# Kernel tuning notes

Measured on AMD Instinct MI355X. Metric: run time of the kernel, lower is better.

## Reference

```python
import jax, jax.numpy as jnp
import numpy as np

HEADS = 8
BN_EPS = 1e-5

def _bn(x2d, g, b):
    # torch BatchNorm1d in training mode: biased batch stats
    mu = x2d.mean(0)
    var = x2d.var(0)
    return (x2d - mu) * jax.lax.rsqrt(var + BN_EPS) * g + b

def _window_indices(H):
    # exclusive-end box coordinates, in the exact order of the torch loop
    m = H // 2
    r0, r1, c0, c1 = [], [], [], []
    for i in range(1, m + 1):
        wins = [(m - i, m + i + 1, m - i, m + i + 1),  # full square
                (m - i, m + 1,     m - i, m + i + 1),  # top half
                (m,     m + i + 1, m - i, m + i + 1),  # bottom half
                (m - i, m + i + 1, m - i, m + 1),      # left half
                (m - i, m + i + 1, m,     m + i + 1)]  # right half
        for a, b, c, d in wins:
            r0.append(a); r1.append(b); c0.append(c); c1.append(d)
    r0 = np.array(r0); r1 = np.array(r1); c0 = np.array(c0); c1 = np.array(c1)
    counts = ((r1 - r0) * (c1 - c0)).astype(np.float32)
    return r0, r1, c0, c1, counts

def _box_sums(P, r0, r1, c0, c1):
    # P: padded 2D prefix sum [B, C, H+1, H+1]; returns [B, C, K]
    return P[:, :, r1, c1] - P[:, :, r0, c1] - P[:, :, r1, c0] + P[:, :, r0, c0]

def _integral(img):
    return jnp.pad(jnp.cumsum(jnp.cumsum(img, axis=2), axis=3), ((0, 0), (0, 0), (1, 0), (1, 0)))

def setup_inputs() -> dict:
    key = jax.random.key(0)
    ks = jax.random.split(key, 8)
    B, Cin, H = 64, 512, 31
    C = 512  # heads * base_dim
    x = jax.random.normal(ks[0], (B, Cin, H, H), dtype=jnp.float32)
    w_v = jax.random.normal(ks[1], (Cin, C), dtype=jnp.float32) * 0.02
    w_k = jax.random.normal(ks[2], (Cin, C), dtype=jnp.float32) * 0.02
    w_fc = jax.random.normal(ks[3], (Cin + C, 512), dtype=jnp.float32) * 0.02
    z = lambda n: jnp.zeros((n,), jnp.float32)
    o = lambda n: jnp.ones((n,), jnp.float32)
    return {"x": x,
            "w_v": w_v, "b_v": z(C), "g_vn": o(C), "b_vn": z(C),
            "w_k": w_k, "b_k": z(C), "g_kn": o(C), "b_kn": z(C),
            "w_fc": w_fc, "b_fc": z(512), "g_fcn": o(512), "b_fcn": z(512)}

def reference(x, w_v, b_v, g_vn, b_vn, w_k, b_k, g_kn, b_kn, w_fc, b_fc, g_fcn, b_fcn):
    B, Cin, H, W = x.shape
    N = H * W
    C = w_v.shape[1]
    d = C // HEADS
    m = H // 2
    xt = x.reshape(B, Cin, N).transpose(0, 2, 1)       # [B, N, Cin]
    x0 = xt[:, N // 2, :]                              # [B, Cin] center pixel feature
    flat = xt.reshape(B * N, Cin)
    v = jax.nn.relu(_bn(flat @ w_v + b_v, g_vn, b_vn))
    v = v.reshape(B, N, C).transpose(0, 2, 1).reshape(B, C, H, H)
    k = _bn(flat @ w_k + b_k, g_kn, b_kn).reshape(B, N, HEADS, d).transpose(0, 2, 1, 3)  # [B,h,N,d]
    q = k[:, :, N // 2, :]                             # [B, h, d]
    attn = jax.nn.softmax(jnp.einsum('bhd,bhnd->bhn', q, k) * (d ** -0.5), axis=-1)      # [B,h,N]
    attn_full = jnp.broadcast_to(attn[:, :, None, :], (B, HEADS, d, N)).reshape(B, C, H, H)
    xw = attn_full * v                                 # attn-weighted values [B,C,H,H]
    eps = 1e-16
    r0, r1, c0, c1, counts = _window_indices(H)
    Px = _integral(xw)
    Pa = _integral(attn_full)
    mx = _box_sums(Px, r0, r1, c0, c1) / counts        # window means of xw   [B,C,K]
    ma = _box_sums(Pa, r0, r1, c0, c1) / counts        # window means of attn [B,C,K]
    y_win = (mx / (ma + eps)).transpose(0, 2, 1)       # [B, K, C]
    y = jnp.concatenate([xw[:, :, m, m][:, None, :], y_win], axis=1)  # [B, n, C]
    # F.normalize(p=2, dim=2)
    y = y / jnp.maximum(jnp.linalg.norm(y, axis=2, keepdims=True), 1e-12)
    n = y.shape[1]
    yy = jnp.concatenate([jnp.broadcast_to(x0[:, None, :], (B, n, Cin)), y], axis=-1)
    out = jax.nn.relu(_bn(yy.reshape(B * n, Cin + C) @ w_fc + b_fc, g_fcn, b_fcn))
    return out.reshape(B, n, -1)
```

## Files before the change

kernel.cpp:

```cpp
#include <hip/hip_runtime.h>
#include <stdint.h>

#define DEV __device__ __forceinline__

typedef __bf16 bf16x8 __attribute__((ext_vector_type(8)));
typedef unsigned short u16x8 __attribute__((ext_vector_type(8)));
typedef float f32x4 __attribute__((ext_vector_type(4)));

DEV uint16_t f2bf(float f) {
    union { float f; uint32_t u; } v; v.f = f;
    uint32_t r = v.u + 0x7fffu + ((v.u >> 16) & 1u);
    return (uint16_t)(r >> 16);
}
DEV float bf2f(uint16_t h) {
    union { uint32_t u; float f; } v; v.u = ((uint32_t)h) << 16;
    return v.f;
}

#if __has_builtin(__builtin_amdgcn_global_load_lds)
DEV void async16(const uint16_t* g, uint16_t* l) {
    __builtin_amdgcn_global_load_lds(
        (const __attribute__((address_space(1))) uint32_t*)g,
        (__attribute__((address_space(3))) uint32_t*)l, 16, 0, 0);
}
#else
DEV void async16(const uint16_t* g, uint16_t* l) {
    *(u16x8*)l = *(const u16x8*)g;
}
#endif

__global__ void k_convert_x(const float* __restrict__ x, uint16_t* __restrict__ xbt) {
    __shared__ float tile[32][33];
    int b = blockIdx.z;
    int n0 = blockIdx.x * 32;
    int c0 = blockIdx.y * 32;
    int tx = threadIdx.x, ty = threadIdx.y;
    #pragma unroll
    for (int i = 0; i < 4; ++i) {
        int c = c0 + ty + 8 * i;
        int n = n0 + tx;
        float v = 0.f;
        if (n < 961) v = x[((size_t)b * 512 + c) * 961 + n];
        tile[ty + 8 * i][tx] = v;
    }
    __syncthreads();
    #pragma unroll
    for (int i = 0; i < 4; ++i) {
        int n = n0 + ty + 8 * i;
        if (n < 961)
            xbt[((size_t)b * 961 + n) * 512 + c0 + tx] = f2bf(tile[tx][ty + 8 * i]);
    }
}

__global__ void k_convert_wvk(const float* __restrict__ wv, const float* __restrict__ wk,
                              uint16_t* __restrict__ wvkt) {
    int idx = blockIdx.x * 256 + threadIdx.x;
    int j = idx >> 9, k = idx & 511;
    float v = (j < 512) ? wv[(size_t)k * 512 + j] : wk[(size_t)k * 512 + (j - 512)];
    wvkt[idx] = f2bf(v);
}
__global__ void k_convert_wfc(const float* __restrict__ wfc, uint16_t* __restrict__ wfct) {
    int idx = blockIdx.x * 256 + threadIdx.x;
    int j = idx >> 10, k = idx & 1023;
    wfct[idx] = f2bf(wfc[(size_t)k * 512 + j]);
}

template<int K, int EPI>
__global__ __launch_bounds__(256, 2)
void k_gemm(const uint16_t* __restrict__ A, const uint16_t* __restrict__ Bt,
            int M_real,
            uint16_t* __restrict__ out_v, uint16_t* __restrict__ out_k,
            float* __restrict__ out_f,
            float* __restrict__ colsum, float* __restrict__ colsq)
{
    __shared__ __align__(16) uint16_t sbuf[8704];
    __shared__ float sStat[256];
    uint16_t* sA = sbuf;
    uint16_t* sB = sbuf + 4096;

    const int tid = threadIdx.x;
    const int wave = tid >> 6, lane = tid & 63;
    const int quad = lane >> 4, l16 = lane & 15;
    int m0, j0;
    if constexpr (EPI == 0) {
        int lin = blockIdx.x;
        int xcd = lin & 7, rest = lin >> 3;
        int jb = rest & 7, mhi = rest >> 3;
        int mb = mhi * 8 + xcd;
        if (mb >= 481) return;
        m0 = mb * 128; j0 = jb * 128;
    } else {
        m0 = blockIdx.y * 128; j0 = blockIdx.x * 128;
    }
    const int wm = wave >> 1, wj = wave & 1;

    const f32x4 fzero = {0.f, 0.f, 0.f, 0.f};
    f32x4 acc[4][4];
    #pragma unroll
    for (int i = 0; i < 4; ++i)
        #pragma unroll
        for (int j = 0; j < 4; ++j) acc[i][j] = fzero;

    const int c0 = tid;
    const int mA0 = c0 >> 2, kq0 = c0 & 3;
    const int c1 = tid + 256;
    const int mA1 = c1 >> 2, kq1 = c1 & 3;

    const int KT = K / 32;
    for (int kt = 0; kt < KT; ++kt) {
        const uint16_t* Ak = A + (size_t)m0 * K + kt * 32;
        const uint16_t* Bk = Bt + (size_t)j0 * K + kt * 32;
        async16(Ak + (size_t)mA0 * K + kq0 * 8, &sA[c0 * 8]);
        async16(Bk + (size_t)mA0 * K + kq0 * 8, &sB[c0 * 8]);
        async16(Ak + (size_t)mA1 * K + kq1 * 8, &sA[c1 * 8]);
        async16(Bk + (size_t)mA1 * K + kq1 * 8, &sB[c1 * 8]);
        __syncthreads();
        bf16x8 af[4], bfr[4];
        #pragma unroll
        for (int i = 0; i < 4; ++i) {
            int m = wm * 64 + i * 16 + l16;
            u16x8 r = *(const u16x8*)&sA[m * 32 + quad * 8];
            af[i] = __builtin_bit_cast(bf16x8, r);
        }
        #pragma unroll
        for (int j = 0; j < 4; ++j) {
            int jj = wj * 64 + j * 16 + l16;
            u16x8 r = *(const u16x8*)&sB[jj * 32 + quad * 8];
            bfr[j] = __builtin_bit_cast(bf16x8, r);
        }
        #pragma unroll
        for (int i = 0; i < 4; ++i)
            #pragma unroll
            for (int j = 0; j < 4; ++j)
                acc[i][j] = __builtin_amdgcn_mfma_f32_16x16x32_bf16(af[i], bfr[j], acc[i][j], 0, 0, 0);
        __syncthreads();
    }

    sStat[tid] = 0.f;
    __syncthreads();

    #pragma unroll
    for (int j = 0; j < 4; ++j) {
        const int col_local = wj * 64 + j * 16 + l16;
        const int jg = j0 + col_local;
        float ls = 0.f, lq = 0.f;
        #pragma unroll
        for (int i = 0; i < 4; ++i) {
            const int rbase = m0 + wm * 64 + i * 16 + quad * 4;
            #pragma unroll
            for (int reg = 0; reg < 4; ++reg) {
                const int r = rbase + reg;
                const float val = acc[i][j][reg];
                if (r < M_real) {
                    ls += val; lq += val * val;
                    if constexpr (EPI == 1) {
                        out_f[(size_t)r * 512 + jg] = val;
                    }
                }
            }
        }
        ls += __shfl_xor(ls, 16); lq += __shfl_xor(lq, 16);
        ls += __shfl_xor(ls, 32); lq += __shfl_xor(lq, 32);
        if (quad == 0) {
            atomicAdd(&sStat[col_local], ls);
            atomicAdd(&sStat[128 + col_local], lq);
        }
    }
    __syncthreads();
    if (tid < 128) atomicAdd(&colsum[j0 + tid], sStat[tid]);
    else           atomicAdd(&colsq[j0 + (tid & 127)], sStat[tid]);

    if constexpr (EPI == 0) {
        const int rr = tid & 127;
        const int cbase = tid >> 7;
        const int r = m0 + rr;
        const bool ok = r < M_real;
        const unsigned bb_ = (unsigned)r / 961u;
        const unsigned nn = (unsigned)r - bb_ * 961u;
        #pragma unroll
        for (int ch = 0; ch < 2; ++ch) {
            if (wj == ch) {
                #pragma unroll
                for (int j = 0; j < 4; ++j) {
                    const int c = j * 16 + l16;
                    #pragma unroll
                    for (int i = 0; i < 4; ++i) {
                        const int rloc = wm * 64 + i * 16 + quad * 4;
                        union { uint16_t h[4]; uint64_t u; } p;
                        #pragma unroll
                        for (int reg = 0; reg < 4; ++reg) p.h[reg] = f2bf(acc[i][j][reg]);
                        *(uint64_t*)&sbuf[c * 136 + rloc] = p.u;
                    }
                }
            }
            __syncthreads();
            #pragma unroll
            for (int it = 0; it < 32; ++it) {
                const int c = cbase + it * 2;
                const int jg = j0 + ch * 64 + c;
                const uint16_t hv = sbuf[c * 136 + rr];
                if (ok) {
                    if (jg < 512) out_v[((size_t)bb_ * 512 + jg) * 961 + nn] = hv;
                    else          out_k[((size_t)bb_ * 512 + (jg - 512)) * 961 + nn] = hv;
                }
            }
            __syncthreads();
        }
    }
}

__global__ void k_bnfin(const float* __restrict__ s, const float* __restrict__ q,
                        const float* __restrict__ g, const float* __restrict__ be,
                        float* __restrict__ a, float* __restrict__ b2, float invM) {
    int j = blockIdx.x * 256 + threadIdx.x;
    float mean = s[j] * invM;
    float var = q[j] * invM - mean * mean;
    float aa = g[j] * rsqrtf(var + 1e-5f);
    a[j] = aa;
    b2[j] = be[j] - mean * aa;
}

__global__ void k_attn(const uint16_t* __restrict__ kraw,
                       const float* __restrict__ avec, const float* __restrict__ bvec,
                       float* __restrict__ attn, float* __restrict__ maw)
{
    __shared__ float qa[64];
    __shared__ float s_qb;
    __shared__ float att[961];
    __shared__ float red[8];

    int bh = blockIdx.x;
    int b = bh >> 3, h = bh & 7;
    int tid = threadIdx.x;

    if (tid < 64) {
        int c = h * 64 + tid;
        float kr = bf2f(kraw[((size_t)b * 512 + c) * 961 + 480]);
        float a = avec[512 + c], bb = bvec[512 + c];
        float qv = kr * a + bb;
        qa[tid] = qv * a;
        float qb = qv * bb;
        for (int off = 32; off; off >>= 1) qb += __shfl_down(qb, off);
        if (tid == 0) s_qb = qb;
    }
    __syncthreads();

    float lg[4];
    float lmax = -1e30f;
    #pragma unroll
    for (int it = 0; it < 4; ++it) {
        int n = tid + it * 256;
        float dot = -1e30f;
        if (n < 961) {
            const uint16_t* kp = kraw + ((size_t)b * 512 + h * 64) * 961 + n;
            float acc = 0.f;
            #pragma unroll 16
            for (int dd = 0; dd < 64; ++dd)
                acc += qa[dd] * bf2f(kp[(size_t)dd * 961]);
            dot = (acc + s_qb) * 0.125f;
        }
        lg[it] = dot;
        lmax = fmaxf(lmax, dot);
    }
    for (int off = 32; off; off >>= 1) lmax = fmaxf(lmax, __shfl_xor(lmax, off));
    if ((tid & 63) == 0) red[tid >> 6] = lmax;
    __syncthreads();
    float bmax = fmaxf(fmaxf(red[0], red[1]), fmaxf(red[2], red[3]));

    float lsum = 0.f;
    #pragma unroll
    for (int it = 0; it < 4; ++it) {
        int n = tid + it * 256;
        if (n < 961) {
            float e = __expf(lg[it] - bmax);
            lg[it] = e;
            lsum += e;
        }
    }
    for (int off = 32; off; off >>= 1) lsum += __shfl_xor(lsum, off);
    if ((tid & 63) == 0) red[4 + (tid >> 6)] = lsum;
    __syncthreads();
    float inv = 1.f / (red[4] + red[5] + red[6] + red[7]);
    #pragma unroll
    for (int it = 0; it < 4; ++it) {
        int n = tid + it * 256;
        if (n < 961) {
            float v = lg[it] * inv;
            att[n] = v;
            attn[(size_t)bh * 961 + n] = v;
        }
    }
    __syncthreads();

    if (tid < 31) { float s = 0.f; for (int cc = 0; cc < 31; ++cc) { s += att[tid * 31 + cc]; att[tid * 31 + cc] = s; } }
    __syncthreads();
    if (tid < 31) { float s = 0.f; for (int rr = 0; rr < 31; ++rr) { s += att[rr * 31 + tid]; att[rr * 31 + tid] = s; } }
    __syncthreads();

    if (tid < 75) {
        int i = tid / 5 + 1, t = tid % 5;
        const int m = 15;
        int r0, r1, cc0, cc1;
        switch (t) {
            case 0: r0 = m - i; r1 = m + i + 1; cc0 = m - i; cc1 = m + i + 1; break;
            case 1: r0 = m - i; r1 = m + 1;     cc0 = m - i; cc1 = m + i + 1; break;
            case 2: r0 = m;     r1 = m + i + 1; cc0 = m - i; cc1 = m + i + 1; break;
            case 3: r0 = m - i; r1 = m + i + 1; cc0 = m - i; cc1 = m + 1;     break;
            default:r0 = m - i; r1 = m + i + 1; cc0 = m;     cc1 = m + i + 1; break;
        }
        auto S = [&](int r, int c) -> float { return (r < 0 || c < 0) ? 0.f : att[r * 31 + c]; };
        float box = S(r1 - 1, cc1 - 1) - S(r0 - 1, cc1 - 1) - S(r1 - 1, cc0 - 1) + S(r0 - 1, cc0 - 1);
        float cnt = (float)((r1 - r0) * (cc1 - cc0));
        maw[(size_t)bh * 75 + tid] = box / cnt;
    }
}

__global__ void k_winbox(const uint16_t* __restrict__ vraw,
                         const float* __restrict__ avec, const float* __restrict__ bvec,
                         const float* __restrict__ attn, const float* __restrict__ maw,
                         float* __restrict__ y)
{
    __shared__ float xw[961];
    __shared__ float s_center;
    int bc = blockIdx.x;
    int b = bc >> 9, c = bc & 511;
    int h = c >> 6;
    int tid = threadIdx.x;
    float a = avec[c], bb = bvec[c];
    const uint16_t* vp = vraw + (size_t)bc * 961;
    const float* ap = attn + (size_t)(b * 8 + h) * 961;
    for (int n = tid; n < 961; n += 128) {
        float v = fmaxf(bf2f(vp[n]) * a + bb, 0.f);
        xw[n] = v * ap[n];
    }
    __syncthreads();
    if (tid == 0) s_center = xw[480];
    __syncthreads();
    if (tid < 31) { float s = 0.f; for (int cc = 0; cc < 31; ++cc) { s += xw[tid * 31 + cc]; xw[tid * 31 + cc] = s; } }
    __syncthreads();
    if (tid < 31) { float s = 0.f; for (int rr = 0; rr < 31; ++rr) { s += xw[rr * 31 + tid]; xw[rr * 31 + tid] = s; } }
    __syncthreads();
    if (tid < 75) {
        int i = tid / 5 + 1, t = tid % 5;
        const int m = 15;
        int r0, r1, cc0, cc1;
        switch (t) {
            case 0: r0 = m - i; r1 = m + i + 1; cc0 = m - i; cc1 = m + i + 1; break;
            case 1: r0 = m - i; r1 = m + 1;     cc0 = m - i; cc1 = m + i + 1; break;
            case 2: r0 = m;     r1 = m + i + 1; cc0 = m - i; cc1 = m + i + 1; break;
            case 3: r0 = m - i; r1 = m + i + 1; cc0 = m - i; cc1 = m + 1;     break;
            default:r0 = m - i; r1 = m + i + 1; cc0 = m;     cc1 = m + i + 1; break;
        }
        auto S = [&](int r, int cc) -> float { return (r < 0 || cc < 0) ? 0.f : xw[r * 31 + cc]; };
        float box = S(r1 - 1, cc1 - 1) - S(r0 - 1, cc1 - 1) - S(r1 - 1, cc0 - 1) + S(r0 - 1, cc0 - 1);
        float cnt = (float)((r1 - r0) * (cc1 - cc0));
        float mx = box / cnt;
        float ma = maw[(size_t)(b * 8 + h) * 75 + tid];
        y[((size_t)b * 76 + 1 + tid) * 512 + c] = mx / (ma + 1e-16f);
    }
    if (tid == 96) y[((size_t)b * 76) * 512 + c] = s_center;
}

__global__ void k_build_yy(const float* __restrict__ y, const float* __restrict__ x,
                           uint16_t* __restrict__ yy)
{
    __shared__ float red[4];
    int row = blockIdx.x;
    int b = row / 76;
    int tid = threadIdx.x;
    const float* yp = y + (size_t)row * 512;
    float v0 = yp[tid], v1 = yp[tid + 256];
    float ss = v0 * v0 + v1 * v1;
    for (int off = 32; off; off >>= 1) ss += __shfl_xor(ss, off);
    if ((tid & 63) == 0) red[tid >> 6] = ss;
    __syncthreads();
    float tot = red[0] + red[1] + red[2] + red[3];
    float inv = 1.f / fmaxf(sqrtf(tot), 1e-12f);
    uint16_t* op = yy + (size_t)row * 1024;
    op[tid]           = f2bf(x[((size_t)b * 512 + tid) * 961 + 480]);
    op[tid + 256]     = f2bf(x[((size_t)b * 512 + tid + 256) * 961 + 480]);
    op[512 + tid]       = f2bf(v0 * inv);
    op[512 + tid + 256] = f2bf(v1 * inv);
}

__global__ void k_fcout(const float* __restrict__ fcraw, const float* __restrict__ a2,
                        const float* __restrict__ b2, float* __restrict__ out)
{
    size_t idx = (size_t)blockIdx.x * 256 + threadIdx.x;
    if (idx < (size_t)4864 * 512) {
        int j = (int)(idx & 511);
        out[idx] = fmaxf(fcraw[idx] * a2[j] + b2[j], 0.f);
    }
}

extern "C" void kernel_launch(void* const* d_in, const int* in_sizes, int n_in,
                              void* d_out, int out_size, void* d_ws, size_t ws_size,
                              hipStream_t stream)
{
    (void)in_sizes; (void)n_in; (void)out_size; (void)ws_size;
    const float* x    = (const float*)d_in[0];
    const float* w_v  = (const float*)d_in[1];
    const float* g_vn = (const float*)d_in[3];
    const float* b_vn = (const float*)d_in[4];
    const float* w_k  = (const float*)d_in[5];
    const float* g_kn = (const float*)d_in[7];
    const float* b_kn = (const float*)d_in[8];
    const float* w_fc = (const float*)d_in[9];
    const float* g_fcn = (const float*)d_in[11];
    const float* b_fcn = (const float*)d_in[12];
    float* out = (float*)d_out;

    char* base = (char*)d_ws;
    size_t off = 0;
    auto alloc = [&](size_t bytes) -> void* {
        void* p = base + off;
        off += (bytes + 255) & ~(size_t)255;
        return p;
    };
    uint16_t* xbt  = (uint16_t*)alloc((size_t)61568 * 512 * 2);
    uint16_t* wvkt = (uint16_t*)alloc((size_t)1024 * 512 * 2);
    uint16_t* wfct = (uint16_t*)alloc((size_t)512 * 1024 * 2);
    uint16_t* vraw = (uint16_t*)alloc((size_t)64 * 512 * 961 * 2);
    uint16_t* kraw = (uint16_t*)alloc((size_t)64 * 512 * 961 * 2);
    float* stats   = (float*)alloc(3072 * 4);
    float* avec    = (float*)alloc(1024 * 4);
    float* bvec    = (float*)alloc(1024 * 4);
    float* a2      = (float*)alloc(512 * 4);
    float* b2fc    = (float*)alloc(512 * 4);
    float* attn    = (float*)alloc((size_t)64 * 8 * 961 * 4);
    float* maw     = (float*)alloc((size_t)64 * 8 * 75 * 4);
    float* y       = (float*)alloc((size_t)64 * 76 * 512 * 4);
    uint16_t* yy   = (uint16_t*)alloc((size_t)4864 * 1024 * 2);
    float* fcraw   = (float*)alloc((size_t)4864 * 512 * 4);

    hipMemsetAsync(stats, 0, 3072 * 4, stream);
    k_convert_x<<<dim3(31, 16, 64), dim3(32, 8), 0, stream>>>(x, xbt);
    k_convert_wvk<<<2048, 256, 0, stream>>>(w_v, w_k, wvkt);
    k_convert_wfc<<<2048, 256, 0, stream>>>(w_fc, wfct);

    k_gemm<512, 0><<<3904, 256, 0, stream>>>(xbt, wvkt, 61504, vraw, kraw, nullptr,
                                             stats, stats + 1024);
    k_bnfin<<<2, 256, 0, stream>>>(stats,       stats + 1024,       g_vn, b_vn, avec,       bvec,       1.f / 61504.f);
    k_bnfin<<<2, 256, 0, stream>>>(stats + 512, stats + 1024 + 512, g_kn, b_kn, avec + 512, bvec + 512, 1.f / 61504.f);

    k_attn<<<512, 256, 0, stream>>>(kraw, avec, bvec, attn, maw);
    k_winbox<<<64 * 512, 128, 0, stream>>>(vraw, avec, bvec, attn, maw, y);
    k_build_yy<<<4864, 256, 0, stream>>>(y, x, yy);

    k_gemm<1024, 1><<<dim3(4, 38), 256, 0, stream>>>(yy, wfct, 4864, nullptr, nullptr, fcraw,
                                                     stats + 2048, stats + 2560);
    k_bnfin<<<2, 256, 0, stream>>>(stats + 2048, stats + 2560, g_fcn, b_fcn, a2, b2fc, 1.f / 4864.f);
    k_fcout<<<9728, 256, 0, stream>>>(fcraw, a2, b2fc, out);
}
```

Measured before the change: 487.5 us.

## Fuse BN finalize into consumers, merge weight converts, deepen GEMM K-step

Removes the three k_bnfin launches by recomputing BN scale and shift inline in k_attn, k_winbox and k_fcout, and merges the two weight-transpose kernels into one launch. The GEMM now stages 64 K-elements per iteration, which halves the number of barriers, and asks for 4 blocks per CU in launch bounds. k_convert_x writes paired bf16 values and k_build_yy reads the centre pixel from the bf16 transposed copy instead of strided fp32 x. The costs are a doubled LDS footprint in the GEMM, which may limit the higher occupancy target, and redundant BN arithmetic per element in k_fcout.

Result: faster. 436.3 us (-10.5%).

```diff
diff --git a/kernel.cpp b/kernel.cpp
--- a/kernel.cpp
+++ b/kernel.cpp
@@ -44,39 +44,51 @@
         tile[ty + 8 * i][tx] = v;
     }
     __syncthreads();
-    #pragma unroll
-    for (int i = 0; i < 4; ++i) {
-        int n = n0 + ty + 8 * i;
-        if (n < 961)
-            xbt[((size_t)b * 961 + n) * 512 + c0 + tx] = f2bf(tile[tx][ty + 8 * i]);
-    }
-}
-
-__global__ void k_convert_wvk(const float* __restrict__ wv, const float* __restrict__ wk,
-                              uint16_t* __restrict__ wvkt) {
+    int idx = ty * 32 + tx;
+    int c2 = (idx & 15) * 2;
+    int nl = idx >> 4;
+    #pragma unroll
+    for (int i = 0; i < 2; ++i) {
+        int nn = nl + 16 * i;
+        int n = n0 + nn;
+        if (n < 961) {
+            ushort2 val;
+            val.x = f2bf(tile[c2][nn]);
+            val.y = f2bf(tile[c2 + 1][nn]);
+            *(ushort2*)&xbt[((size_t)b * 961 + n) * 512 + c0 + c2] = val;
+        }
+    }
+}
+
+__global__ void k_convert_w(const float* __restrict__ wv, const float* __restrict__ wk,
+                            const float* __restrict__ wfc,
+                            uint16_t* __restrict__ wvkt, uint16_t* __restrict__ wfct) {
     int idx = blockIdx.x * 256 + threadIdx.x;
-    int j = idx >> 9, k = idx & 511;
-    float v = (j < 512) ? wv[(size_t)k * 512 + j] : wk[(size_t)k * 512 + (j - 512)];
-    wvkt[idx] = f2bf(v);
-}
-__global__ void k_convert_wfc(const float* __restrict__ wfc, uint16_t* __restrict__ wfct) {
-    int idx = blockIdx.x * 256 + threadIdx.x;
-    int j = idx >> 10, k = idx & 1023;
-    wfct[idx] = f2bf(wfc[(size_t)k * 512 + j]);
+    if (idx < 524288) {
+        int j = idx >> 9, k = idx & 511;
+        float v = (j < 512) ? wv[(size_t)k * 512 + j] : wk[(size_t)k * 512 + (j - 512)];
+        wvkt[idx] = f2bf(v);
+    } else {
+        int t = idx - 524288;
+        int j = t >> 10, k = t & 1023;
+        wfct[t] = f2bf(wfc[(size_t)k * 512 + j]);
+    }
 }
 
 template<int K, int EPI>
-__global__ __launch_bounds__(256, 2)
+__global__ __launch_bounds__(256, 4)
 void k_gemm(const uint16_t* __restrict__ A, const uint16_t* __restrict__ Bt,
             int M_real,
             uint16_t* __restrict__ out_v, uint16_t* __restrict__ out_k,
             float* __restrict__ out_f,
             float* __restrict__ colsum, float* __restrict__ colsq)
 {
-    __shared__ __align__(16) uint16_t sbuf[8704];
+    __shared__ __align__(16) uint16_t sbuf[16384];
     __shared__ float sStat[256];
-    uint16_t* sA = sbuf;
-    uint16_t* sB = sbuf + 4096;
+    uint16_t* sA0 = sbuf;
+    uint16_t* sA1 = sbuf + 4096;
+    uint16_t* sB0 = sbuf + 8192;
+    uint16_t* sB1 = sbuf + 12288;
 
     const int tid = threadIdx.x;
     const int wave = tid >> 6, lane = tid & 63;
@@ -106,33 +118,42 @@
     const int c1 = tid + 256;
     const int mA1 = c1 >> 2, kq1 = c1 & 3;
 
-    const int KT = K / 32;
+    const int KT = K / 64;
     for (int kt = 0; kt < KT; ++kt) {
-        const uint16_t* Ak = A + (size_t)m0 * K + kt * 32;
-        const uint16_t* Bk = Bt + (size_t)j0 * K + kt * 32;
-        async16(Ak + (size_t)mA0 * K + kq0 * 8, &sA[c0 * 8]);
-        async16(Bk + (size_t)mA0 * K + kq0 * 8, &sB[c0 * 8]);
-        async16(Ak + (size_t)mA1 * K + kq1 * 8, &sA[c1 * 8]);
-        async16(Bk + (size_t)mA1 * K + kq1 * 8, &sB[c1 * 8]);
+        const uint16_t* Ak = A + (size_t)m0 * K + kt * 64;
+        const uint16_t* Bk = Bt + (size_t)j0 * K + kt * 64;
+        async16(Ak + (size_t)mA0 * K + kq0 * 8,      &sA0[c0 * 8]);
+        async16(Ak + (size_t)mA1 * K + kq1 * 8,      &sA0[c1 * 8]);
+        async16(Ak + (size_t)mA0 * K + 32 + kq0 * 8, &sA1[c0 * 8]);
+        async16(Ak + (size_t)mA1 * K + 32 + kq1 * 8, &sA1[c1 * 8]);
+        async16(Bk + (size_t)mA0 * K + kq0 * 8,      &sB0[c0 * 8]);
+        async16(Bk + (size_t)mA1 * K + kq1 * 8,      &sB0[c1 * 8]);
+        async16(Bk + (size_t)mA0 * K + 32 + kq0 * 8, &sB1[c0 * 8]);
+        async16(Bk + (size_t)mA1 * K + 32 + kq1 * 8, &sB1[c1 * 8]);
         __syncthreads();
-        bf16x8 af[4], bfr[4];
         #pragma unroll
-        for (int i = 0; i < 4; ++i) {
-            int m = wm * 64 + i * 16 + l16;
-            u16x8 r = *(const u16x8*)&sA[m * 32 + quad * 8];
-            af[i] = __builtin_bit_cast(bf16x8, r);
-        }
-        #pragma unroll
-        for (int j = 0; j < 4; ++j) {
-            int jj = wj * 64 + j * 16 + l16;
-            u16x8 r = *(const u16x8*)&sB[jj * 32 + quad * 8];
-            bfr[j] = __builtin_bit_cast(bf16x8, r);
-        }
-        #pragma unroll
-        for (int i = 0; i < 4; ++i)
+        for (int p = 0; p < 2; ++p) {
+            const uint16_t* pA = p ? sA1 : sA0;
+            const uint16_t* pB = p ? sB1 : sB0;
+            bf16x8 af[4], bfr[4];
             #pragma unroll
-            for (int j = 0; j < 4; ++j)
-                acc[i][j] = __builtin_amdgcn_mfma_f32_16x16x32_bf16(af[i], bfr[j], acc[i][j], 0, 0, 0);
+            for (int i = 0; i < 4; ++i) {
+                int m = wm * 64 + i * 16 + l16;
+                u16x8 r = *(const u16x8*)&pA[m * 32 + quad * 8];
+                af[i] = __builtin_bit_cast(bf16x8, r);
+            }
+            #pragma unroll
+            for (int j = 0; j < 4; ++j) {
+                int jj = wj * 64 + j * 16 + l16;
+                u16x8 r = *(const u16x8*)&pB[jj * 32 + quad * 8];
+                bfr[j] = __builtin_bit_cast(bf16x8, r);
+            }
+            #pragma unroll
+            for (int i = 0; i < 4; ++i)
+                #pragma unroll
+                for (int j = 0; j < 4; ++j)
+                    acc[i][j] = __builtin_amdgcn_mfma_f32_16x16x32_bf16(af[i], bfr[j], acc[i][j], 0, 0, 0);
+        }
         __syncthreads();
     }
 
@@ -209,19 +230,9 @@
     }
 }
 
-__global__ void k_bnfin(const float* __restrict__ s, const float* __restrict__ q,
-                        const float* __restrict__ g, const float* __restrict__ be,
-                        float* __restrict__ a, float* __restrict__ b2, float invM) {
-    int j = blockIdx.x * 256 + threadIdx.x;
-    float mean = s[j] * invM;
-    float var = q[j] * invM - mean * mean;
-    float aa = g[j] * rsqrtf(var + 1e-5f);
-    a[j] = aa;
-    b2[j] = be[j] - mean * aa;
-}
-
 __global__ void k_attn(const uint16_t* __restrict__ kraw,
-                       const float* __restrict__ avec, const float* __restrict__ bvec,
+                       const float* __restrict__ colsum, const float* __restrict__ colsq,
+                       const float* __restrict__ g_kn, const float* __restrict__ b_kn,
                        float* __restrict__ attn, float* __restrict__ maw)
 {
     __shared__ float qa[64];
@@ -232,11 +243,15 @@
     int bh = blockIdx.x;
     int b = bh >> 3, h = bh & 7;
     int tid = threadIdx.x;
+    constexpr float invM = 1.f / 61504.f;
 
     if (tid < 64) {
         int c = h * 64 + tid;
+        float mean = colsum[512 + c] * invM;
+        float q_ = colsq[512 + c] * invM;
+        float a = g_kn[c] * rsqrtf(q_ - mean * mean + 1e-5f);
+        float bb = b_kn[c] - mean * a;
         float kr = bf2f(kraw[((size_t)b * 512 + c) * 961 + 480]);
-        float a = avec[512 + c], bb = bvec[512 + c];
         float qv = kr * a + bb;
         qa[tid] = qv * a;
         float qb = qv * bb;
@@ -316,7 +331,8 @@
 }
 
 __global__ void k_winbox(const uint16_t* __restrict__ vraw,
-                         const float* __restrict__ avec, const float* __restrict__ bvec,
+                         const float* __restrict__ colsum, const float* __restrict__ colsq,
+                         const float* __restrict__ g_vn, const float* __restrict__ b_vn,
                          const float* __restrict__ attn, const float* __restrict__ maw,
                          float* __restrict__ y)
 {
@@ -326,7 +342,11 @@
     int b = bc >> 9, c = bc & 511;
     int h = c >> 6;
     int tid = threadIdx.x;
-    float a = avec[c], bb = bvec[c];
+    constexpr float invM = 1.f / 61504.f;
+    float mean = colsum[c] * invM;
+    float q_ = colsq[c] * invM;
+    float a = g_vn[c] * rsqrtf(q_ - mean * mean + 1e-5f);
+    float bb = b_vn[c] - mean * a;
     const uint16_t* vp = vraw + (size_t)bc * 961;
     const float* ap = attn + (size_t)(b * 8 + h) * 961;
     for (int n = tid; n < 961; n += 128) {
@@ -361,7 +381,7 @@
     if (tid == 96) y[((size_t)b * 76) * 512 + c] = s_center;
 }
 
-__global__ void k_build_yy(const float* __restrict__ y, const float* __restrict__ x,
+__global__ void k_build_yy(const float* __restrict__ y, const uint16_t* __restrict__ xbt,
                            uint16_t* __restrict__ yy)
 {
     __shared__ float red[4];
@@ -377,19 +397,27 @@
     float tot = red[0] + red[1] + red[2] + red[3];
     float inv = 1.f / fmaxf(sqrtf(tot), 1e-12f);
     uint16_t* op = yy + (size_t)row * 1024;
-    op[tid]           = f2bf(x[((size_t)b * 512 + tid) * 961 + 480]);
-    op[tid + 256]     = f2bf(x[((size_t)b * 512 + tid + 256) * 961 + 480]);
+    const uint16_t* x0p = xbt + ((size_t)b * 961 + 480) * 512;
+    op[tid]           = x0p[tid];
+    op[tid + 256]     = x0p[tid + 256];
     op[512 + tid]       = f2bf(v0 * inv);
     op[512 + tid + 256] = f2bf(v1 * inv);
 }
 
-__global__ void k_fcout(const float* __restrict__ fcraw, const float* __restrict__ a2,
-                        const float* __restrict__ b2, float* __restrict__ out)
+__global__ void k_fcout(const float* __restrict__ fcraw,
+                        const float* __restrict__ colsum, const float* __restrict__ colsq,
+                        const float* __restrict__ g, const float* __restrict__ be,
+                        float* __restrict__ out)
 {
     size_t idx = (size_t)blockIdx.x * 256 + threadIdx.x;
     if (idx < (size_t)4864 * 512) {
         int j = (int)(idx & 511);
-        out[idx] = fmaxf(fcraw[idx] * a2[j] + b2[j], 0.f);
+        constexpr float invM = 1.f / 4864.f;
+        float mean = colsum[j] * invM;
+        float q_ = colsq[j] * invM;
+        float a = g[j] * rsqrtf(q_ - mean * mean + 1e-5f);
+        float bb = be[j] - mean * a;
+        out[idx] = fmaxf(fcraw[idx] * a + bb, 0.f);
     }
 }
 
@@ -423,10 +451,6 @@
     uint16_t* vraw = (uint16_t*)alloc((size_t)64 * 512 * 961 * 2);
     uint16_t* kraw = (uint16_t*)alloc((size_t)64 * 512 * 961 * 2);
     float* stats   = (float*)alloc(3072 * 4);
-    float* avec    = (float*)alloc(1024 * 4);
-    float* bvec    = (float*)alloc(1024 * 4);
-    float* a2      = (float*)alloc(512 * 4);
-    float* b2fc    = (float*)alloc(512 * 4);
     float* attn    = (float*)alloc((size_t)64 * 8 * 961 * 4);
     float* maw     = (float*)alloc((size_t)64 * 8 * 75 * 4);
     float* y       = (float*)alloc((size_t)64 * 76 * 512 * 4);
@@ -435,20 +459,16 @@
 
     hipMemsetAsync(stats, 0, 3072 * 4, stream);
     k_convert_x<<<dim3(31, 16, 64), dim3(32, 8), 0, stream>>>(x, xbt);
-    k_convert_wvk<<<2048, 256, 0, stream>>>(w_v, w_k, wvkt);
-    k_convert_wfc<<<2048, 256, 0, stream>>>(w_fc, wfct);
+    k_convert_w<<<4096, 256, 0, stream>>>(w_v, w_k, w_fc, wvkt, wfct);
 
     k_gemm<512, 0><<<3904, 256, 0, stream>>>(xbt, wvkt, 61504, vraw, kraw, nullptr,
                                              stats, stats + 1024);
-    k_bnfin<<<2, 256, 0, stream>>>(stats,       stats + 1024,       g_vn, b_vn, avec,       bvec,       1.f / 61504.f);
-    k_bnfin<<<2, 256, 0, stream>>>(stats + 512, stats + 1024 + 512, g_kn, b_kn, avec + 512, bvec + 512, 1.f / 61504.f);
-
-    k_attn<<<512, 256, 0, stream>>>(kraw, avec, bvec, attn, maw);
-    k_winbox<<<64 * 512, 128, 0, stream>>>(vraw, avec, bvec, attn, maw, y);
-    k_build_yy<<<4864, 256, 0, stream>>>(y, x, yy);
+
+    k_attn<<<512, 256, 0, stream>>>(kraw, stats, stats + 1024, g_kn, b_kn, attn, maw);
+    k_winbox<<<64 * 512, 128, 0, stream>>>(vraw, stats, stats + 1024, g_vn, b_vn, attn, maw, y);
+    k_build_yy<<<4864, 256, 0, stream>>>(y, xbt, yy);
 
     k_gemm<1024, 1><<<dim3(4, 38), 256, 0, stream>>>(yy, wfct, 4864, nullptr, nullptr, fcraw,
                                                      stats + 2048, stats + 2560);
-    k_bnfin<<<2, 256, 0, stream>>>(stats + 2048, stats + 2560, g_fcn, b_fcn, a2, b2fc, 1.f / 4864.f);
-    k_fcout<<<9728, 256, 0, stream>>>(fcraw, a2, b2fc, out);
-}
+    k_fcout<<<9728, 256, 0, stream>>>(fcraw, stats + 2048, stats + 2560, g_fcn, b_fcn, out);
+}
```
